# Optimization experiments

Measured on AMD Instinct MI355X. Metric: run time of the kernel, lower is better.

The kernel has to match this reference:

```python
import jax, jax.numpy as jnp
import numpy as np

HIDDEN, DOWN, UP, NH, RHD = 2048, 512, 1024, 16, 64
HEAD_DIM = HIDDEN // NH        # 128 (used only in the score scale)
V_HEAD = UP // NH              # 64
BASE = 10000.0


def _rope(q):
    # q: [bs, heads, seq, d] with even d. Faithful to the torch module,
    # including its swapped sin/cos cache names.
    d = q.shape[-1]
    seq = q.shape[2]
    theta = BASE ** (-jnp.arange(0, d, 2, dtype=jnp.float32) / d)      # [d/2]
    pos = jnp.arange(seq, dtype=jnp.float32)[:, None] * theta[None, :]  # [seq, d/2]
    cos_pos = jnp.repeat(jnp.sin(pos), 2, axis=-1)  # torch code: cos_pos = sin(...)
    sin_pos = jnp.repeat(jnp.cos(pos), 2, axis=-1)  # torch code: sin_pos = cos(...)
    q2 = jnp.stack([-q[..., 1::2], q[..., ::2]], axis=-1).reshape(q.shape)
    return q * cos_pos[None, None] + q2 * sin_pos[None, None]


def setup_inputs() -> dict:
    key = jax.random.key(0)
    ks = jax.random.split(key, 12)
    bs, seq = 16, 512

    def lin(k, fan_in, fan_out):
        kw, kb = jax.random.split(k)
        bound = 1.0 / np.sqrt(fan_in)
        W = jax.random.uniform(kw, (fan_in, fan_out), jnp.float32, -bound, bound)
        b = jax.random.uniform(kb, (fan_out,), jnp.float32, -bound, bound)
        return W, b

    x = jax.random.normal(ks[0], (bs, seq, HIDDEN), jnp.float32)
    mask = jax.random.randint(ks[1], (bs, seq), 0, 2, jnp.int32)
    w_dkv, b_dkv = lin(ks[2], HIDDEN, DOWN)
    w_dq, b_dq = lin(ks[3], HIDDEN, DOWN)
    w_uq, b_uq = lin(ks[4], DOWN, UP)
    w_uk, b_uk = lin(ks[5], DOWN, UP)
    w_uv, b_uv = lin(ks[6], DOWN, UP)
    w_qr, b_qr = lin(ks[7], DOWN, RHD * NH)
    w_kr, b_kr = lin(ks[8], DOWN, RHD)
    w_fc, b_fc = lin(ks[9], NH * V_HEAD, HIDDEN)
    return dict(x=x, mask=mask, w_dkv=w_dkv, b_dkv=b_dkv, w_dq=w_dq, b_dq=b_dq,
                w_uq=w_uq, b_uq=b_uq, w_uk=w_uk, b_uk=b_uk, w_uv=w_uv, b_uv=b_uv,
                w_qr=w_qr, b_qr=b_qr, w_kr=w_kr, b_kr=b_kr, w_fc=w_fc, b_fc=b_fc)


def reference(x, mask, w_dkv, b_dkv, w_dq, b_dq, w_uq, b_uq, w_uk, b_uk,
              w_uv, b_uv, w_qr, b_qr, w_kr, b_kr, w_fc, b_fc):
    bs, seq, _ = x.shape
    # latent down-projections
    c_kv = x @ w_dkv + b_dkv                       # [bs, seq, DOWN]
    c_q = x @ w_dq + b_dq                          # [bs, seq, DOWN]
    # content up-projections
    k_c = (c_kv @ w_uk + b_uk).reshape(bs, seq, NH, UP // NH).transpose(0, 2, 1, 3)
    v_c = (c_kv @ w_uv + b_uv).reshape(bs, seq, NH, V_HEAD).transpose(0, 2, 1, 3)
    q_c = (c_q @ w_uq + b_uq).reshape(bs, seq, NH, UP // NH).transpose(0, 2, 1, 3)
    # rope branches
    q_r = (c_q @ w_qr + b_qr).reshape(bs, seq, NH, RHD).transpose(0, 2, 1, 3)
    q_r = _rope(q_r)                               # [bs, NH, seq, RHD]
    k_r = (c_kv @ w_kr + b_kr)[:, None]            # [bs, 1, seq, RHD]
    k_r = _rope(k_r)
    # concat content + rope dims
    q = jnp.concatenate([q_c, q_r], axis=-1)                        # [bs,NH,seq,UP/NH+RHD]
    k = jnp.concatenate([k_c, jnp.broadcast_to(k_r, (bs, NH, seq, RHD))], axis=-1)
    scale = 1.0 / (HEAD_DIM ** 0.5 + RHD ** 0.5)
    scores = jnp.einsum('bhqd,bhkd->bhqk', q, k) * scale
    scores = jnp.where(mask[:, None, None, :] == 0, -jnp.inf, scores)
    attn = jax.nn.softmax(scores, axis=-1)
    ctx = jnp.einsum('bhqk,bhkd->bhqd', attn, v_c)                  # [bs,NH,seq,V_HEAD]
    ctx = ctx.transpose(0, 2, 1, 3).reshape(bs, seq, NH * V_HEAD)
    return ctx @ w_fc + b_fc
```

## Files before the change

### kernel.cpp

```cpp
#include <hip/hip_runtime.h>
#include <cstdint>
#include <cmath>

typedef unsigned short u16;
typedef unsigned int   u32;
typedef _Float16 f16x8 __attribute__((ext_vector_type(8)));
typedef float f32x4  __attribute__((ext_vector_type(4)));

#define MFMAH(a, b, c) __builtin_amdgcn_mfma_f32_16x16x32_f16((a), (b), (c), 0, 0, 0)

__device__ __forceinline__ u16 f2h(float f) {
  _Float16 h = (_Float16)f;
  return __builtin_bit_cast(u16, h);
}
__device__ __forceinline__ float h2f(u16 u) {
  return (float)__builtin_bit_cast(_Float16, u);
}
__device__ __forceinline__ float fexp2(float x) { return __builtin_amdgcn_exp2f(x); }
__device__ __forceinline__ void async16(const void* g, void* l) {
  __builtin_amdgcn_global_load_lds((const __attribute__((address_space(1))) u32*)g,
                                   (__attribute__((address_space(3))) u32*)l, 16, 0, 0);
}

__global__ void prep_kernel(float2* __restrict__ stab,
                            const float* __restrict__ buq, const float* __restrict__ bqr,
                            const float* __restrict__ buk, const float* __restrict__ buv,
                            const float* __restrict__ bkr,
                            float* __restrict__ biasQ, float* __restrict__ biasKV) {
  int idx = blockIdx.x * 256 + threadIdx.x;
  if (idx < 16384) {
    int s = idx >> 5, i = idx & 31;
    float theta = exp2f((float)i * (-13.287712379549449f / 32.0f));
    float ang = (float)s * theta;
    stab[idx] = make_float2(sinf(ang), cosf(ang));
  }
  int j = idx - 16384;
  if (j >= 0 && j < 2048) biasQ[j] = (j < 1024) ? buq[j] : bqr[j - 1024];
  int k = idx - 18432;
  if (k >= 0 && k < 2176)
    biasKV[k] = (k < 1024) ? buk[k]
              : (k < 2048) ? buv[k - 1024]
              : (k < 2112) ? bkr[k - 2048] : 0.f;
}

__global__ void convert_x_kernel(const float* __restrict__ x, u16* __restrict__ xh, int n4) {
  int i = blockIdx.x * blockDim.x + threadIdx.x;
  if (i >= n4) return;
  float4 v = reinterpret_cast<const float4*>(x)[i];
  uint2 p;
  p.x = (u32)f2h(v.x) | ((u32)f2h(v.y) << 16);
  p.y = (u32)f2h(v.z) | ((u32)f2h(v.w) << 16);
  reinterpret_cast<uint2*>(xh)[i] = p;
}

struct Wptrs { const float* w0; const float* w1; const float* w2; const float* w3; };
template <int NOUT>
__global__ void wtrans_kernel(Wptrs wp, int N,
                              u16* __restrict__ Thi, u16* __restrict__ Tlo,
                              int row_off0, int row_stride, int dst_ld) {
  __shared__ float tile[32][33];
  const float* W = (blockIdx.z == 0) ? wp.w0 : (blockIdx.z == 1) ? wp.w1
                 : (blockIdx.z == 2) ? wp.w2 : wp.w3;
  int row_off = row_off0 + blockIdx.z * row_stride;
  int k0 = blockIdx.x * 32, n0 = blockIdx.y * 32;
  int tx = threadIdx.x & 31, ty = threadIdx.x >> 5;
#pragma unroll
  for (int i = 0; i < 32; i += 8)
    tile[ty + i][tx] = W[(size_t)(k0 + ty + i) * N + n0 + tx];
  __syncthreads();
#pragma unroll
  for (int i = 0; i < 32; i += 8) {
    float v = tile[tx][ty + i];
    size_t o = (size_t)(row_off + n0 + ty + i) * dst_ld + k0 + tx;
    u16 h = f2h(v);
    Thi[o] = h;
    if constexpr (NOUT == 2) Tlo[o] = f2h(v - h2f(h));
  }
}

template <int MODE, int TERMS>
__global__ __launch_bounds__(256, TERMS == 2 ? 3 : 4) void gemmh_kernel(
    const u16* __restrict__ Ah, int lda,
    const u16* __restrict__ Bhi, const u16* __restrict__ Blo, int ldb,
    const float* __restrict__ bias, const float* __restrict__ bias2, int bsplit,
    void* __restrict__ out0, void* __restrict__ out1, void* __restrict__ out2,
    const float2* __restrict__ stab, int N, int K, int ldc) {
  __shared__ u16 lA[128 * 64];
  __shared__ u16 lB[TERMS][128 * 64];
  const int tid = threadIdx.x;
  const int wave = tid >> 6, lane = tid & 63;
  const int lrow = lane & 15, kgrp = lane >> 4;
  const int nwg = gridDim.x * gridDim.y;
  const int orig = blockIdx.y * gridDim.x + blockIdx.x;
  const int swz = (orig & 7) * (nwg >> 3) + (orig >> 3);
  const int bm = (swz % gridDim.x) * 128, bn = (swz / gridDim.x) * 128;
  const int wm = (wave >> 1) * 64, wn = (wave & 1) * 64;
  const int srow = lane >> 3, sg = lane & 7;

  f32x4 acc[4][4];
  const f32x4 zero = {0.f, 0.f, 0.f, 0.f};
#pragma unroll
  for (int i = 0; i < 4; ++i)
#pragma unroll
    for (int j = 0; j < 4; ++j) acc[i][j] = zero;

  for (int kt = 0; kt < K; kt += 64) {
#pragma unroll
    for (int ii = 0; ii < 4; ++ii) {
      int inst = wave * 4 + ii;
      int row = inst * 8 + srow;
      int koff = kt + ((sg ^ (row & 7)) << 3);
      async16(Ah + (size_t)(bm + row) * lda + koff, &lA[inst * 512]);
      int brow = bn + row;
      if (brow > N - 1) brow = N - 1;
      async16(Bhi + (size_t)brow * ldb + koff, &lB[0][inst * 512]);
      if constexpr (TERMS == 2)
        async16(Blo + (size_t)brow * ldb + koff, &lB[TERMS - 1][inst * 512]);
    }
    asm volatile("s_waitcnt vmcnt(0)" ::: "memory");
    __syncthreads();

#pragma unroll
    for (int ks = 0; ks < 2; ++ks) {
      f16x8 ah[4], b0v[4], b1v[4];
#pragma unroll
      for (int mi = 0; mi < 4; ++mi) {
        int row = wm + mi * 16 + lrow;
        int off = row * 128 + ((ks * 64 + kgrp * 16) ^ ((row & 7) << 4));
        ah[mi] = *(const f16x8*)((const char*)lA + off);
      }
#pragma unroll
      for (int ni = 0; ni < 4; ++ni) {
        int row = wn + ni * 16 + lrow;
        int off = row * 128 + ((ks * 64 + kgrp * 16) ^ ((row & 7) << 4));
        b0v[ni] = *(const f16x8*)((const char*)lB[0] + off);
        if constexpr (TERMS == 2)
          b1v[ni] = *(const f16x8*)((const char*)lB[TERMS - 1] + off);
      }
#pragma unroll
      for (int mi = 0; mi < 4; ++mi)
#pragma unroll
        for (int ni = 0; ni < 4; ++ni) {
          acc[mi][ni] = MFMAH(ah[mi], b0v[ni], acc[mi][ni]);
          if constexpr (TERMS == 2)
            acc[mi][ni] = MFMAH(ah[mi], b1v[ni], acc[mi][ni]);
        }
    }
    __syncthreads();
  }

#pragma unroll
  for (int mi = 0; mi < 4; ++mi) {
#pragma unroll
    for (int ni = 0; ni < 4; ++ni) {
      int col = bn + wn + ni * 16 + lrow;
      float bv = (col < bsplit) ? bias[col] : bias2[col - bsplit];
      int row0 = bm + wm + mi * 16 + kgrp * 4;
      if constexpr (MODE == 0) {
#pragma unroll
        for (int r = 0; r < 4; ++r)
          ((float*)out0)[(size_t)(row0 + r) * ldc + col] = acc[mi][ni][r] + bv;
      } else if constexpr (MODE == 3) {
#pragma unroll
        for (int r = 0; r < 4; ++r)
          ((u16*)out0)[(size_t)(row0 + r) * ldc + col] = f2h(acc[mi][ni][r] + bv);
      } else if constexpr (MODE == 7) {
        if (col < 1024) {
#pragma unroll
          for (int r = 0; r < 4; ++r) {
            int row = row0 + r;
            ((u16*)out0)[(((size_t)((row >> 9) * 16 + (col >> 6)) * 512 + (row & 511)) << 7)
                         + (col & 63)] = f2h(acc[mi][ni][r] + bv);
          }
        } else {
          int cc = col - 1024, hh = cc >> 6, d = cc & 63, i2 = d >> 1;
          bool odd = d & 1;
#pragma unroll
          for (int r = 0; r < 4; ++r) {
            int row = row0 + r, s = row & 511;
            float vv = acc[mi][ni][r] + bv;
            float p = __shfl_xor(vv, 1, 64);
            float2 t2 = stab[s * 32 + i2];
            float o = odd ? (vv * t2.x + p * t2.y) : (vv * t2.x - p * t2.y);
            ((u16*)out0)[(((size_t)((row >> 9) * 16 + hh) * 512 + (row & 511)) << 7)
                         + 64 + d] = f2h(o);
          }
        }
      } else if constexpr (MODE == 6) {
        if (col < 1024) {
#pragma unroll
          for (int r = 0; r < 4; ++r) {
            int row = row0 + r;
            ((u16*)out0)[(((size_t)((row >> 9) * 16 + (col >> 6)) * 512 + (row & 511)) << 7)
                         + (col & 63)] = f2h(acc[mi][ni][r] + bv);
          }
        } else if (col < 2048) {
          int cc = col - 1024;
          u16 h0 = f2h(acc[mi][ni][0] + bv), h1 = f2h(acc[mi][ni][1] + bv);
          u16 h2 = f2h(acc[mi][ni][2] + bv), h3 = f2h(acc[mi][ni][3] + bv);
          uint2 pk2;
          pk2.x = (u32)h0 | ((u32)h1 << 16);
          pk2.y = (u32)h2 | ((u32)h3 << 16);
          size_t base = ((size_t)((row0 >> 9) * 16 + (cc >> 6)) * 64 + (cc & 63)) * 512
                        + (row0 & 511);
          *reinterpret_cast<uint2*>((u16*)out1 + base) = pk2;
        } else {
#pragma unroll
          for (int r = 0; r < 4; ++r)
            ((float*)out2)[(size_t)(row0 + r) * 128 + (col - 2048)] = acc[mi][ni][r] + bv;
        }
      }
    }
  }
}

__global__ void ropek_kernel(const float* __restrict__ kr, const float2* __restrict__ stab,
                             u16* __restrict__ Kb) {
  int idx = blockIdx.x * 256 + threadIdx.x;
  int t = idx >> 5, i = idx & 31;
  float vx = kr[(size_t)t * 128 + 2 * i], vy = kr[(size_t)t * 128 + 2 * i + 1];
  float2 t2 = stab[(t & 511) * 32 + i];
  float o0 = vx * t2.x - vy * t2.y;
  float o1 = vy * t2.x + vx * t2.y;
  u32 pk2 = (u32)f2h(o0) | ((u32)f2h(o1) << 16);
  int bb = t >> 9, ss = t & 511;
  size_t base = (size_t)bb * 16 * 512 * 128;
#pragma unroll
  for (int hh = 0; hh < 16; ++hh)
    *reinterpret_cast<u32*>(Kb + base + ((size_t)(hh * 512 + ss)) * 128 + 64 + 2 * i) = pk2;
}

__global__ __launch_bounds__(256, 4) void attn_kernel(
    const u16* __restrict__ Qb, const u16* __restrict__ Kb, const u16* __restrict__ Vt,
    const int* __restrict__ mask, u16* __restrict__ ctx,
    float scale2) {
  __shared__ u16 sQ[64 * 128];
  __shared__ u16 sK[64 * 128];
  __shared__ u16 sV[64 * 64];
  const int tid = threadIdx.x, wave = tid >> 6, lane = tid & 63;
  const int lrow = lane & 15, g = lane >> 4;
  const int bh = blockIdx.x, b = bh >> 4, h = bh & 15;
  const int q0 = blockIdx.y * 64;
  const size_t qkbase = (size_t)bh * 512 * 128;
  const size_t vbase = (size_t)bh * 64 * 512;

  {
    int gg = lane & 15, rr = lane >> 4;
#pragma unroll
    for (int ii = 0; ii < 4; ++ii) {
      int inst = wave * 4 + ii;
      int row = inst * 4 + rr;
      int perm = (gg & 8) | ((gg & 7) ^ (row & 7));
      async16(Qb + qkbase + (size_t)(q0 + row) * 128 + perm * 8, &sQ[inst * 512]);
    }
  }

  const f32x4 zero = {0.f, 0.f, 0.f, 0.f};
  f32x4 O[4];
#pragma unroll
  for (int nf = 0; nf < 4; ++nf) O[nf] = zero;
  float m_run = -1e30f, lsum = 0.f;

  const int laneA = lrow + ((lane & 16) << 1);
  const int laneB = laneA + 16;
  const bool sel = (lane & 32) != 0;

  for (int kvt = 0; kvt < 8; ++kvt) {
    const int kv0 = kvt * 64;
    {
      int gg = lane & 15, rr = lane >> 4;
#pragma unroll
      for (int ii = 0; ii < 4; ++ii) {
        int inst = wave * 4 + ii;
        int row = inst * 4 + rr;
        int perm = (gg & 8) | ((gg & 7) ^ (row & 7));
        async16(Kb + qkbase + (size_t)(kv0 + row) * 128 + perm * 8, &sK[inst * 512]);
      }
      int g2 = lane & 7, r2 = lane >> 3;
#pragma unroll
      for (int ii = 0; ii < 2; ++ii) {
        int inst = wave * 2 + ii;
        int row = inst * 8 + r2;
        async16(Vt + vbase + (size_t)row * 512 + kv0 + ((g2 ^ (row & 7)) << 3),
                &sV[inst * 512]);
      }
    }
    float mb[4][4];
#pragma unroll
    for (int nf = 0; nf < 4; ++nf) {
      int4 mk = *reinterpret_cast<const int4*>(&mask[b * 512 + kv0 + nf * 16 + g * 4]);
      mb[nf][0] = mk.x ? 0.f : -1e30f;
      mb[nf][1] = mk.y ? 0.f : -1e30f;
      mb[nf][2] = mk.z ? 0.f : -1e30f;
      mb[nf][3] = mk.w ? 0.f : -1e30f;
    }

    asm volatile("s_waitcnt vmcnt(0)" ::: "memory");
    __syncthreads();

    f32x4 S[4];
#pragma unroll
    for (int nf = 0; nf < 4; ++nf) S[nf] = zero;
#pragma unroll
    for (int ks = 0; ks < 4; ++ks) {
      int qrow = wave * 16 + lrow;
      int kb = ks * 64 + g * 16;
      f16x8 bq = *(const f16x8*)((const char*)sQ + qrow * 256 + (kb ^ ((qrow & 7) << 4)));
#pragma unroll
      for (int nf = 0; nf < 4; ++nf) {
        int krow = nf * 16 + lrow;
        f16x8 ak = *(const f16x8*)((const char*)sK + krow * 256 + (kb ^ ((krow & 7) << 4)));
        S[nf] = MFMAH(ak, bq, S[nf]);
      }
    }

    float pvv[4][4];
    float tm = -1e30f;
#pragma unroll
    for (int nf = 0; nf < 4; ++nf) {
#pragma unroll
      for (int r = 0; r < 4; ++r) {
        float v = fmaf(S[nf][r], scale2, mb[nf][r]);
        pvv[nf][r] = v;
        tm = fmaxf(tm, v);
      }
    }
    tm = fmaxf(tm, __shfl_xor(tm, 16, 64));
    tm = fmaxf(tm, __shfl_xor(tm, 32, 64));

    u32 pk[4][2];
    float ts = 0.f;
    bool grow = tm > m_run + 8.f;
    if (__any(grow ? 1 : 0)) {
      float newm = fmaxf(m_run, tm);
      float sc = fexp2(m_run - newm);
      m_run = newm;
#pragma unroll
      for (int nf = 0; nf < 4; ++nf) {
        float e0 = fexp2(pvv[nf][0] - newm), e1 = fexp2(pvv[nf][1] - newm);
        float e2 = fexp2(pvv[nf][2] - newm), e3 = fexp2(pvv[nf][3] - newm);
        ts += (e0 + e1) + (e2 + e3);
        pk[nf][0] = (u32)f2h(e0) | ((u32)f2h(e1) << 16);
        pk[nf][1] = (u32)f2h(e2) | ((u32)f2h(e3) << 16);
      }
      lsum = lsum * sc + ts;
      float scq[4];
#pragma unroll
      for (int r = 0; r < 4; ++r) scq[r] = __shfl(sc, g * 4 + r, 64);
#pragma unroll
      for (int nf = 0; nf < 4; ++nf)
#pragma unroll
        for (int r = 0; r < 4; ++r) O[nf][r] *= scq[r];
    } else {
#pragma unroll
      for (int nf = 0; nf < 4; ++nf) {
        float e0 = fexp2(pvv[nf][0] - m_run), e1 = fexp2(pvv[nf][1] - m_run);
        float e2 = fexp2(pvv[nf][2] - m_run), e3 = fexp2(pvv[nf][3] - m_run);
        ts += (e0 + e1) + (e2 + e3);
        pk[nf][0] = (u32)f2h(e0) | ((u32)f2h(e1) << 16);
        pk[nf][1] = (u32)f2h(e2) | ((u32)f2h(e3) << 16);
      }
      lsum += ts;
    }

#pragma unroll
    for (int ks = 0; ks < 2; ++ks) {
      int n0 = 2 * ks, n1 = 2 * ks + 1;
      u32 w0a = (u32)__shfl((int)pk[n0][0], laneA, 64);
      u32 w0b = (u32)__shfl((int)pk[n1][0], laneA, 64);
      u32 w1a = (u32)__shfl((int)pk[n0][1], laneA, 64);
      u32 w1b = (u32)__shfl((int)pk[n1][1], laneA, 64);
      u32 w2a = (u32)__shfl((int)pk[n0][0], laneB, 64);
      u32 w2b = (u32)__shfl((int)pk[n1][0], laneB, 64);
      u32 w3a = (u32)__shfl((int)pk[n0][1], laneB, 64);
      u32 w3b = (u32)__shfl((int)pk[n1][1], laneB, 64);
      union { u32 w[4]; f16x8 v; } ap;
      ap.w[0] = sel ? w0b : w0a;
      ap.w[1] = sel ? w1b : w1a;
      ap.w[2] = sel ? w2b : w2a;
      ap.w[3] = sel ? w3b : w3a;
      int kb = ks * 64 + g * 16;
#pragma unroll
      for (int nf = 0; nf < 4; ++nf) {
        int vr = nf * 16 + lrow;
        f16x8 bv = *(const f16x8*)((const char*)sV + vr * 128 + (kb ^ ((vr & 7) << 4)));
        O[nf] = MFMAH(ap.v, bv, O[nf]);
      }
    }
    __syncthreads();
  }

  lsum += __shfl_xor(lsum, 16, 64);
  lsum += __shfl_xor(lsum, 32, 64);
  float linv[4];
#pragma unroll
  for (int r = 0; r < 4; ++r) linv[r] = 1.0f / __shfl(lsum, g * 4 + r, 64);

#pragma unroll
  for (int r = 0; r < 4; ++r) {
    int trow = b * 512 + q0 + wave * 16 + g * 4 + r;
#pragma unroll
    for (int nf = 0; nf < 4; ++nf) {
      int col = h * 64 + nf * 16 + lrow;
      ctx[(size_t)trow * 1024 + col] = f2h(O[nf][r] * linv[r]);
    }
  }
}

extern "C" void kernel_launch(void* const* d_in, const int* in_sizes, int n_in,
                              void* d_out, int out_size, void* d_ws, size_t ws_size,
                              hipStream_t stream) {
  const float* x     = (const float*)d_in[0];
  const int*   mask  = (const int*)d_in[1];
  const float* w_dkv = (const float*)d_in[2];
  const float* b_dkv = (const float*)d_in[3];
  const float* w_dq  = (const float*)d_in[4];
  const float* b_dq  = (const float*)d_in[5];
  const float* w_uq  = (const float*)d_in[6];
  const float* b_uq  = (const float*)d_in[7];
  const float* w_uk  = (const float*)d_in[8];
  const float* b_uk  = (const float*)d_in[9];
  const float* w_uv  = (const float*)d_in[10];
  const float* b_uv  = (const float*)d_in[11];
  const float* w_qr  = (const float*)d_in[12];
  const float* b_qr  = (const float*)d_in[13];
  const float* w_kr  = (const float*)d_in[14];
  const float* b_kr  = (const float*)d_in[15];
  const float* w_fc  = (const float*)d_in[16];
  const float* b_fc  = (const float*)d_in[17];
  float* out = (float*)d_out;

  char* ws = (char*)d_ws;
  size_t off = 0;
  auto alloc = [&](size_t bytes) -> void* {
    void* p = ws + off;
    off += (bytes + 255) & ~(size_t)255;
    return p;
  };
  u16* xh     = (u16*)alloc(33554432);
  u16* WfTh   = (u16*)alloc(4194304);
  u16* WfTl   = (u16*)alloc(4194304);
  u16* WqT    = (u16*)alloc(2097152);
  u16* WkvT   = (u16*)alloc(2228224);
  u16* WfcTh  = (u16*)alloc(4194304);
  u16* WfcTl  = (u16*)alloc(4194304);
  u16* c      = (u16*)alloc(16777216);
  u16* Qb     = (u16*)alloc(33554432);
  u16* Kb     = (u16*)alloc(33554432);
  u16* Vt     = (u16*)alloc(16777216);
  float* krf  = (float*)alloc(4194304);
  float2* stab = (float2*)alloc(131072);
  float* biasQ  = (float*)alloc(8192);
  float* biasKV = (float*)alloc(8704);
  u16* ctx = c;
  (void)ws_size; (void)in_sizes; (void)n_in; (void)out_size;

  const float scale = 1.0f / (sqrtf(128.0f) + sqrtf(64.0f));
  const float scale2 = scale * 1.4426950408889634f;

  prep_kernel<<<81, 256, 0, stream>>>(stab, b_uq, b_qr, b_uk, b_uv, b_kr, biasQ, biasKV);
  convert_x_kernel<<<16384, 256, 0, stream>>>(x, xh, 4194304);
  {
    Wptrs wf{w_dkv, w_dq, nullptr, nullptr};
    wtrans_kernel<2><<<dim3(64, 16, 2), 256, 0, stream>>>(wf, 512, WfTh, WfTl, 0, 512, 2048);
    Wptrs wq{w_uq, w_qr, nullptr, nullptr};
    wtrans_kernel<1><<<dim3(16, 32, 2), 256, 0, stream>>>(wq, 1024, WqT, nullptr, 0, 1024, 512);
    Wptrs wkv{w_uk, w_uv, nullptr, nullptr};
    wtrans_kernel<1><<<dim3(16, 32, 2), 256, 0, stream>>>(wkv, 1024, WkvT, nullptr, 0, 1024, 512);
    Wptrs wkr{w_kr, nullptr, nullptr, nullptr};
    wtrans_kernel<1><<<dim3(16, 2, 1), 256, 0, stream>>>(wkr, 64, WkvT, nullptr, 2048, 0, 512);
    Wptrs wfc{w_fc, nullptr, nullptr, nullptr};
    wtrans_kernel<2><<<dim3(32, 64, 1), 256, 0, stream>>>(wfc, 2048, WfcTh, WfcTl, 0, 0, 1024);
  }

  gemmh_kernel<3, 2><<<dim3(64, 8), 256, 0, stream>>>(
      xh, 2048, WfTh, WfTl, 2048, b_dkv, b_dq, 512,
      (void*)c, nullptr, nullptr, nullptr, 1024, 2048, 1024);
  gemmh_kernel<7, 1><<<dim3(64, 16), 256, 0, stream>>>(
      c + 512, 1024, WqT, nullptr, 512, biasQ, biasQ, 2048,
      (void*)Qb, nullptr, nullptr, stab, 2048, 512, 0);
  gemmh_kernel<6, 1><<<dim3(64, 17), 256, 0, stream>>>(
      c, 1024, WkvT, nullptr, 512, biasKV, biasKV, 2176,
      (void*)Kb, (void*)Vt, (void*)krf, nullptr, 2176, 512, 0);

  ropek_kernel<<<1024, 256, 0, stream>>>(krf, stab, Kb);

  attn_kernel<<<dim3(256, 8), 256, 0, stream>>>(Qb, Kb, Vt, mask, ctx, scale2);

  gemmh_kernel<0, 2><<<dim3(64, 16), 256, 0, stream>>>(
      ctx, 1024, WfcTh, WfcTl, 1024, b_fc, b_fc, 2048,
      (void*)out, nullptr, nullptr, nullptr, 2048, 1024, 2048);
}
```

Before: 448.6 us.

## Drop split-fp16 weight low terms and fuse k rope into KV GEMM epilogue

Removes the hi/lo two-term fp16 weight split for the down-projection and output GEMMs, halving their MFMA work and B-tile loads and raising occupancy to 4 blocks per CU. Also folds the k rope rotation and its 16-way head broadcast into the KV GEMM epilogue, eliminating the separate ropek kernel and the fp32 intermediate buffer. The cost is lower weight precision (plain fp16), which could raise numerical error against the fp32 reference, plus a heavier epilogue in one GEMM.

```diff
diff --git a/kernel.cpp b/kernel.cpp
--- a/kernel.cpp
+++ b/kernel.cpp
@@ -54,9 +54,7 @@
 }
 
 struct Wptrs { const float* w0; const float* w1; const float* w2; const float* w3; };
-template <int NOUT>
-__global__ void wtrans_kernel(Wptrs wp, int N,
-                              u16* __restrict__ Thi, u16* __restrict__ Tlo,
+__global__ void wtrans_kernel(Wptrs wp, int N, u16* __restrict__ Thi,
                               int row_off0, int row_stride, int dst_ld) {
   __shared__ float tile[32][33];
   const float* W = (blockIdx.z == 0) ? wp.w0 : (blockIdx.z == 1) ? wp.w1
@@ -69,24 +67,19 @@
     tile[ty + i][tx] = W[(size_t)(k0 + ty + i) * N + n0 + tx];
   __syncthreads();
 #pragma unroll
-  for (int i = 0; i < 32; i += 8) {
-    float v = tile[tx][ty + i];
-    size_t o = (size_t)(row_off + n0 + ty + i) * dst_ld + k0 + tx;
-    u16 h = f2h(v);
-    Thi[o] = h;
-    if constexpr (NOUT == 2) Tlo[o] = f2h(v - h2f(h));
-  }
-}
-
-template <int MODE, int TERMS>
-__global__ __launch_bounds__(256, TERMS == 2 ? 3 : 4) void gemmh_kernel(
+  for (int i = 0; i < 32; i += 8)
+    Thi[(size_t)(row_off + n0 + ty + i) * dst_ld + k0 + tx] = f2h(tile[tx][ty + i]);
+}
+
+template <int MODE>
+__global__ __launch_bounds__(256, 4) void gemmh_kernel(
     const u16* __restrict__ Ah, int lda,
-    const u16* __restrict__ Bhi, const u16* __restrict__ Blo, int ldb,
+    const u16* __restrict__ Bh, int ldb,
     const float* __restrict__ bias, const float* __restrict__ bias2, int bsplit,
-    void* __restrict__ out0, void* __restrict__ out1, void* __restrict__ out2,
+    void* __restrict__ out0, void* __restrict__ out1,
     const float2* __restrict__ stab, int N, int K, int ldc) {
   __shared__ u16 lA[128 * 64];
-  __shared__ u16 lB[TERMS][128 * 64];
+  __shared__ u16 lB[128 * 64];
   const int tid = threadIdx.x;
   const int wave = tid >> 6, lane = tid & 63;
   const int lrow = lane & 15, kgrp = lane >> 4;
@@ -113,16 +106,14 @@
       async16(Ah + (size_t)(bm + row) * lda + koff, &lA[inst * 512]);
       int brow = bn + row;
       if (brow > N - 1) brow = N - 1;
-      async16(Bhi + (size_t)brow * ldb + koff, &lB[0][inst * 512]);
-      if constexpr (TERMS == 2)
-        async16(Blo + (size_t)brow * ldb + koff, &lB[TERMS - 1][inst * 512]);
+      async16(Bh + (size_t)brow * ldb + koff, &lB[inst * 512]);
     }
     asm volatile("s_waitcnt vmcnt(0)" ::: "memory");
     __syncthreads();
 
 #pragma unroll
     for (int ks = 0; ks < 2; ++ks) {
-      f16x8 ah[4], b0v[4], b1v[4];
+      f16x8 ah[4], bv[4];
 #pragma unroll
       for (int mi = 0; mi < 4; ++mi) {
         int row = wm + mi * 16 + lrow;
@@ -133,18 +124,13 @@
       for (int ni = 0; ni < 4; ++ni) {
         int row = wn + ni * 16 + lrow;
         int off = row * 128 + ((ks * 64 + kgrp * 16) ^ ((row & 7) << 4));
-        b0v[ni] = *(const f16x8*)((const char*)lB[0] + off);
-        if constexpr (TERMS == 2)
-          b1v[ni] = *(const f16x8*)((const char*)lB[TERMS - 1] + off);
+        bv[ni] = *(const f16x8*)((const char*)lB + off);
       }
 #pragma unroll
       for (int mi = 0; mi < 4; ++mi)
 #pragma unroll
-        for (int ni = 0; ni < 4; ++ni) {
-          acc[mi][ni] = MFMAH(ah[mi], b0v[ni], acc[mi][ni]);
-          if constexpr (TERMS == 2)
-            acc[mi][ni] = MFMAH(ah[mi], b1v[ni], acc[mi][ni]);
-        }
+        for (int ni = 0; ni < 4; ++ni)
+          acc[mi][ni] = MFMAH(ah[mi], bv[ni], acc[mi][ni]);
     }
     __syncthreads();
   }
@@ -154,23 +140,23 @@
 #pragma unroll
     for (int ni = 0; ni < 4; ++ni) {
       int col = bn + wn + ni * 16 + lrow;
-      float bv = (col < bsplit) ? bias[col] : bias2[col - bsplit];
+      float bv2 = (col < bsplit) ? bias[col] : bias2[col - bsplit];
       int row0 = bm + wm + mi * 16 + kgrp * 4;
       if constexpr (MODE == 0) {
 #pragma unroll
         for (int r = 0; r < 4; ++r)
-          ((float*)out0)[(size_t)(row0 + r) * ldc + col] = acc[mi][ni][r] + bv;
+          ((float*)out0)[(size_t)(row0 + r) * ldc + col] = acc[mi][ni][r] + bv2;
       } else if constexpr (MODE == 3) {
 #pragma unroll
         for (int r = 0; r < 4; ++r)
-          ((u16*)out0)[(size_t)(row0 + r) * ldc + col] = f2h(acc[mi][ni][r] + bv);
+          ((u16*)out0)[(size_t)(row0 + r) * ldc + col] = f2h(acc[mi][ni][r] + bv2);
       } else if constexpr (MODE == 7) {
         if (col < 1024) {
 #pragma unroll
           for (int r = 0; r < 4; ++r) {
             int row = row0 + r;
             ((u16*)out0)[(((size_t)((row >> 9) * 16 + (col >> 6)) * 512 + (row & 511)) << 7)
-                         + (col & 63)] = f2h(acc[mi][ni][r] + bv);
+                         + (col & 63)] = f2h(acc[mi][ni][r] + bv2);
           }
         } else {
           int cc = col - 1024, hh = cc >> 6, d = cc & 63, i2 = d >> 1;
@@ -178,7 +164,7 @@
 #pragma unroll
           for (int r = 0; r < 4; ++r) {
             int row = row0 + r, s = row & 511;
-            float vv = acc[mi][ni][r] + bv;
+            float vv = acc[mi][ni][r] + bv2;
             float p = __shfl_xor(vv, 1, 64);
             float2 t2 = stab[s * 32 + i2];
             float o = odd ? (vv * t2.x + p * t2.y) : (vv * t2.x - p * t2.y);
@@ -192,42 +178,38 @@
           for (int r = 0; r < 4; ++r) {
             int row = row0 + r;
             ((u16*)out0)[(((size_t)((row >> 9) * 16 + (col >> 6)) * 512 + (row & 511)) << 7)
-                         + (col & 63)] = f2h(acc[mi][ni][r] + bv);
+                         + (col & 63)] = f2h(acc[mi][ni][r] + bv2);
           }
         } else if (col < 2048) {
           int cc = col - 1024;
-          u16 h0 = f2h(acc[mi][ni][0] + bv), h1 = f2h(acc[mi][ni][1] + bv);
-          u16 h2 = f2h(acc[mi][ni][2] + bv), h3 = f2h(acc[mi][ni][3] + bv);
+          u16 h0 = f2h(acc[mi][ni][0] + bv2), h1 = f2h(acc[mi][ni][1] + bv2);
+          u16 h2 = f2h(acc[mi][ni][2] + bv2), h3 = f2h(acc[mi][ni][3] + bv2);
           uint2 pk2;
           pk2.x = (u32)h0 | ((u32)h1 << 16);
           pk2.y = (u32)h2 | ((u32)h3 << 16);
           size_t base = ((size_t)((row0 >> 9) * 16 + (cc >> 6)) * 64 + (cc & 63)) * 512
                         + (row0 & 511);
           *reinterpret_cast<uint2*>((u16*)out1 + base) = pk2;
-        } else {
-#pragma unroll
-          for (int r = 0; r < 4; ++r)
-            ((float*)out2)[(size_t)(row0 + r) * 128 + (col - 2048)] = acc[mi][ni][r] + bv;
+        } else if (col < 2112) {
+          int d = col - 2048, i2 = d >> 1;
+          bool odd = d & 1;
+#pragma unroll
+          for (int r = 0; r < 4; ++r) {
+            int row = row0 + r, s = row & 511;
+            float vv = acc[mi][ni][r] + bv2;
+            float p = __shfl_xor(vv, 1, 64);
+            float2 t2 = stab[s * 32 + i2];
+            float o = odd ? (vv * t2.x + p * t2.y) : (vv * t2.x - p * t2.y);
+            u16 oh = f2h(o);
+            size_t base = (size_t)(row >> 9) * 16 * 512 * 128;
+#pragma unroll
+            for (int hh = 0; hh < 16; ++hh)
+              ((u16*)out0)[base + ((size_t)(hh * 512 + s) << 7) + 64 + d] = oh;
+          }
         }
       }
     }
   }
-}
-
-__global__ void ropek_kernel(const float* __restrict__ kr, const float2* __restrict__ stab,
-                             u16* __restrict__ Kb) {
-  int idx = blockIdx.x * 256 + threadIdx.x;
-  int t = idx >> 5, i = idx & 31;
-  float vx = kr[(size_t)t * 128 + 2 * i], vy = kr[(size_t)t * 128 + 2 * i + 1];
-  float2 t2 = stab[(t & 511) * 32 + i];
-  float o0 = vx * t2.x - vy * t2.y;
-  float o1 = vy * t2.x + vx * t2.y;
-  u32 pk2 = (u32)f2h(o0) | ((u32)f2h(o1) << 16);
-  int bb = t >> 9, ss = t & 511;
-  size_t base = (size_t)bb * 16 * 512 * 128;
-#pragma unroll
-  for (int hh = 0; hh < 16; ++hh)
-    *reinterpret_cast<u32*>(Kb + base + ((size_t)(hh * 512 + ss)) * 128 + 64 + 2 * i) = pk2;
 }
 
 __global__ __launch_bounds__(256, 4) void attn_kernel(
@@ -438,17 +420,14 @@
     return p;
   };
   u16* xh     = (u16*)alloc(33554432);
-  u16* WfTh   = (u16*)alloc(4194304);
-  u16* WfTl   = (u16*)alloc(4194304);
+  u16* WfT    = (u16*)alloc(4194304);
   u16* WqT    = (u16*)alloc(2097152);
   u16* WkvT   = (u16*)alloc(2228224);
-  u16* WfcTh  = (u16*)alloc(4194304);
-  u16* WfcTl  = (u16*)alloc(4194304);
+  u16* WfcT   = (u16*)alloc(4194304);
   u16* c      = (u16*)alloc(16777216);
   u16* Qb     = (u16*)alloc(33554432);
   u16* Kb     = (u16*)alloc(33554432);
   u16* Vt     = (u16*)alloc(16777216);
-  float* krf  = (float*)alloc(4194304);
   float2* stab = (float2*)alloc(131072);
   float* biasQ  = (float*)alloc(8192);
   float* biasKV = (float*)alloc(8704);
@@ -462,32 +441,30 @@
   convert_x_kernel<<<16384, 256, 0, stream>>>(x, xh, 4194304);
   {
     Wptrs wf{w_dkv, w_dq, nullptr, nullptr};
-    wtrans_kernel<2><<<dim3(64, 16, 2), 256, 0, stream>>>(wf, 512, WfTh, WfTl, 0, 512, 2048);
+    wtrans_kernel<<<dim3(64, 16, 2), 256, 0, stream>>>(wf, 512, WfT, 0, 512, 2048);
     Wptrs wq{w_uq, w_qr, nullptr, nullptr};
-    wtrans_kernel<1><<<dim3(16, 32, 2), 256, 0, stream>>>(wq, 1024, WqT, nullptr, 0, 1024, 512);
+    wtrans_kernel<<<dim3(16, 32, 2), 256, 0, stream>>>(wq, 1024, WqT, 0, 1024, 512);
     Wptrs wkv{w_uk, w_uv, nullptr, nullptr};
-    wtrans_kernel<1><<<dim3(16, 32, 2), 256, 0, stream>>>(wkv, 1024, WkvT, nullptr, 0, 1024, 512);
+    wtrans_kernel<<<dim3(16, 32, 2), 256, 0, stream>>>(wkv, 1024, WkvT, 0, 1024, 512);
     Wptrs wkr{w_kr, nullptr, nullptr, nullptr};
-    wtrans_kernel<1><<<dim3(16, 2, 1), 256, 0, stream>>>(wkr, 64, WkvT, nullptr, 2048, 0, 512);
+    wtrans_kernel<<<dim3(16, 2, 1), 256, 0, stream>>>(wkr, 64, WkvT, 2048, 0, 512);
     Wptrs wfc{w_fc, nullptr, nullptr, nullptr};
-    wtrans_kernel<2><<<dim3(32, 64, 1), 256, 0, stream>>>(wfc, 2048, WfcTh, WfcTl, 0, 0, 1024);
-  }
-
-  gemmh_kernel<3, 2><<<dim3(64, 8), 256, 0, stream>>>(
-      xh, 2048, WfTh, WfTl, 2048, b_dkv, b_dq, 512,
-      (void*)c, nullptr, nullptr, nullptr, 1024, 2048, 1024);
-  gemmh_kernel<7, 1><<<dim3(64, 16), 256, 0, stream>>>(
-      c + 512, 1024, WqT, nullptr, 512, biasQ, biasQ, 2048,
-      (void*)Qb, nullptr, nullptr, stab, 2048, 512, 0);
-  gemmh_kernel<6, 1><<<dim3(64, 17), 256, 0, stream>>>(
-      c, 1024, WkvT, nullptr, 512, biasKV, biasKV, 2176,
-      (void*)Kb, (void*)Vt, (void*)krf, nullptr, 2176, 512, 0);
-
-  ropek_kernel<<<1024, 256, 0, stream>>>(krf, stab, Kb);
+    wtrans_kernel<<<dim3(32, 64, 1), 256, 0, stream>>>(wfc, 2048, WfcT, 0, 0, 1024);
+  }
+
+  gemmh_kernel<3><<<dim3(64, 8), 256, 0, stream>>>(
+      xh, 2048, WfT, 2048, b_dkv, b_dq, 512,
+      (void*)c, nullptr, nullptr, 1024, 2048, 1024);
+  gemmh_kernel<7><<<dim3(64, 16), 256, 0, stream>>>(
+      c + 512, 1024, WqT, 512, biasQ, biasQ, 2048,
+      (void*)Qb, nullptr, stab, 2048, 512, 0);
+  gemmh_kernel<6><<<dim3(64, 17), 256, 0, stream>>>(
+      c, 1024, WkvT, 512, biasKV, biasKV, 2176,
+      (void*)Kb, (void*)Vt, stab, 2176, 512, 0);
 
   attn_kernel<<<dim3(256, 8), 256, 0, stream>>>(Qb, Kb, Vt, mask, ctx, scale2);
 
-  gemmh_kernel<0, 2><<<dim3(64, 16), 256, 0, stream>>>(
-      ctx, 1024, WfcTh, WfcTl, 1024, b_fc, b_fc, 2048,
-      (void*)out, nullptr, nullptr, nullptr, 2048, 1024, 2048);
-}
+  gemmh_kernel<0><<<dim3(64, 16), 256, 0, stream>>>(
+      ctx, 1024, WfcT, 1024, b_fc, b_fc, 2048,
+      (void*)out, nullptr, nullptr, 2048, 1024, 2048);
+}
```

Result: no change. 441.7 us (-1.5%).
